# Optimization experiments

Measured on AMD Instinct MI355X. Metric: run time of the kernel, lower is better.

Reference implementation:

```python
import jax, jax.numpy as jnp
import numpy as np

N, D, DB, E, H = 1024, 512, 64, 32768, 1024

def setup_inputs() -> dict:
    key = jax.random.key(0)
    k = jax.random.split(key, 6)
    object_feats = jax.random.normal(k[0], (N, D), dtype=jnp.float32)
    bboxes_embedding = jax.random.normal(k[1], (N, N, DB), dtype=jnp.float32)
    pairs = jax.random.randint(k[2], (E, 2), 0, N, dtype=jnp.int64)
    # Kaiming-normal-ish init for the two Linear layers
    W1 = jax.random.normal(k[3], (D + D + DB, H), dtype=jnp.float32) * np.sqrt(2.0 / (D + D + DB))
    b1 = jnp.zeros((H,), dtype=jnp.float32)
    W2 = jax.random.normal(k[4], (H, D), dtype=jnp.float32) * np.sqrt(2.0 / H)
    b2 = jnp.zeros((D,), dtype=jnp.float32)
    return {"object_feats": object_feats, "bboxes_embedding": bboxes_embedding,
            "pairs": pairs, "W1": W1, "b1": b1, "W2": W2, "b2": b2}

def reference(object_feats, bboxes_embedding, pairs, W1, b1, W2, b2):
    sub = pairs[:, 0]
    obj = pairs[:, 1]
    # gather pair features: [E, D] each, plus pairwise bbox embedding [E, DB]
    f_sub = object_feats[sub]
    f_obj = object_feats[obj]
    bb = bboxes_embedding[sub, obj]
    x = jnp.concatenate((f_sub, f_obj, bb), axis=1)  # [E, 2D+DB]
    h = jax.nn.relu(x @ W1 + b1)
    out = h @ W2 + b2  # [E, D]
    n = object_feats.shape[0]
    # scatter-mean into subject nodes; each node's own feature is included once,
    # so new_feat[i] = (object_feats[i] + sum_{pairs with sub==i} out) / (1 + count[i]).
    # Nodes with no incident pairs keep their original feature (count==0 -> identity).
    seg_sum = jax.ops.segment_sum(out, sub, num_segments=n)  # [N, D]
    count = jax.ops.segment_sum(jnp.ones((out.shape[0],), dtype=out.dtype), sub, num_segments=n)
    new_feats = (object_feats + seg_sum) / (1.0 + count)[:, None]
    return (new_feats, bboxes_embedding, pairs)
```

## Files before the change

### kernel.cpp

```cpp
#include <hip/hip_runtime.h>

#define N_OBJ 1024
#define E_P   32768

typedef float f32x4 __attribute__((ext_vector_type(4)));
typedef short bf16x8 __attribute__((ext_vector_type(8)));
typedef unsigned short u16x4 __attribute__((ext_vector_type(4)));

__device__ __forceinline__ unsigned short f2bf(float f) {
    unsigned u = __float_as_uint(f);
    u = u + 0x7FFFu + ((u >> 16) & 1u);
    return (unsigned short)(u >> 16);
}

#define OFF_A    0
#define LEN_A    2097152
#define OFF_SCAN (OFF_A + LEN_A)
#define LEN_SCAN 1048576
#define OFF_PQ   (OFF_SCAN + LEN_SCAN)
#define LEN_PQ   3145728
#define OFF_SEG  (OFF_PQ + LEN_PQ)
#define LEN_SEG  7340032
#define OFF_OUT  (OFF_SEG + LEN_SEG)
#define LEN_OUT  3145728

__device__ __forceinline__ void copy_role(const float4* __restrict__ src,
                                          float4* __restrict__ dst,
                                          int off, int len, int nb, int cb) {
    int stride = nb * 256;
    int i = off + cb * 256 + threadIdx.x;
    int end = off + len;
    for (; i + stride < end; i += 2 * stride) {
        float4 a = src[i];
        float4 b = src[i + stride];
        dst[i] = a;
        dst[i + stride] = b;
    }
    if (i < end) dst[i] = src[i];
}

__global__ __launch_bounds__(256) void k_a(const float* __restrict__ W1,
                                           const float* __restrict__ W2,
                                           const float* __restrict__ feats,
                                           const int* __restrict__ pairs,
                                           unsigned short* __restrict__ w1pqT,
                                           unsigned short* __restrict__ w1cT,
                                           unsigned short* __restrict__ w2T,
                                           unsigned short* __restrict__ featsb,
                                           float* __restrict__ out_pairs,
                                           int* __restrict__ counts,
                                           const float4* __restrict__ csrc,
                                           float4* __restrict__ cdst) {
    int bid = blockIdx.x, tid = threadIdx.x;
    if ((bid % 3) == 2) { copy_role(csrc, cdst, OFF_A, LEN_A, 1056, bid / 3); return; }
    int job = (bid / 3) * 2 + (bid % 3);
    if (job >= 1856) {
        int i = (job - 1856) * 256 + tid;
        out_pairs[i] = (float)pairs[i];
        if (i < E_P) atomicAdd(&counts[pairs[2 * i]], 1);
        return;
    }
    if (job >= 1600) {
        int base = (job - 1600) * 2048 + tid * 8;
        float4 v0 = *(const float4*)&feats[base];
        float4 v1 = *(const float4*)&feats[base + 4];
        u16x4 o0 = { f2bf(v0.x), f2bf(v0.y), f2bf(v0.z), f2bf(v0.w) };
        u16x4 o1 = { f2bf(v1.x), f2bf(v1.y), f2bf(v1.z), f2bf(v1.w) };
        *(u16x4*)&featsb[base] = o0;
        *(u16x4*)&featsb[base + 4] = o1;
        return;
    }
    const float* in; unsigned short* out;
    int LDI, LDO, r0, c0, nbase, kbase;
    if (job < 1024) {
        r0 = (job >> 5) * 32; c0 = (job & 31) * 32;
        in = W1; LDI = 1024; out = w1pqT; LDO = 512;
        nbase = c0 + (r0 >= 512 ? 1024 : 0); kbase = r0 & 511;
    } else if (job < 1088) {
        int t = job - 1024; r0 = 1024 + (t >> 5) * 32; c0 = (t & 31) * 32;
        in = W1; LDI = 1024; out = w1cT; LDO = 64;
        nbase = c0; kbase = r0 - 1024;
    } else {
        int t = job - 1088; r0 = (t >> 4) * 32; c0 = (t & 15) * 32;
        in = W2; LDI = 512; out = w2T; LDO = 1024;
        nbase = c0; kbase = r0;
    }
    __shared__ float lds[32][33];
    int ti = tid >> 3, tj = (tid & 7) * 4;
    float4 v = *(const float4*)&in[(size_t)(r0 + ti) * LDI + c0 + tj];
    lds[ti][tj] = v.x; lds[ti][tj + 1] = v.y; lds[ti][tj + 2] = v.z; lds[ti][tj + 3] = v.w;
    __syncthreads();
    int oc = tid >> 3, oj = (tid & 7) * 4;
    u16x4 o = { f2bf(lds[oj][oc]), f2bf(lds[oj + 1][oc]),
                f2bf(lds[oj + 2][oc]), f2bf(lds[oj + 3][oc]) };
    *(u16x4*)&out[(size_t)(nbase + oc) * LDO + kbase + oj] = o;
}

__global__ __launch_bounds__(256) void k_scan(const int* __restrict__ counts,
                                              int* __restrict__ cursor,
                                              unsigned* __restrict__ brec,
                                              int* __restrict__ bcnt,
                                              const float4* __restrict__ csrc,
                                              float4* __restrict__ cdst) {
    int bid = blockIdx.x, tid = threadIdx.x;
    if (bid != 0) { copy_role(csrc, cdst, OFF_SCAN, LEN_SCAN, 1024, bid - 1); return; }
    __shared__ int buf[2][256];
    int c[4]; int s = 0;
    #pragma unroll
    for (int i = 0; i < 4; ++i) { c[i] = counts[tid * 4 + i]; s += c[i]; }
    buf[0][tid] = s;
    __syncthreads();
    int sel = 0;
    for (int d = 1; d < 256; d <<= 1) {
        int v = buf[sel][tid];
        if (tid >= d) v += buf[sel][tid - d];
        buf[sel ^ 1][tid] = v;
        sel ^= 1;
        __syncthreads();
    }
    int base = buf[sel][tid] - s;
    int run = base;
    #pragma unroll
    for (int i = 0; i < 4; ++i) { cursor[tid * 4 + i] = run; run += c[i]; }
    int nb[4]; int t = 0;
    #pragma unroll
    for (int i = 0; i < 4; ++i) { nb[i] = (c[i] + 31) >> 5; t += nb[i]; }
    __syncthreads();
    buf[0][tid] = t;
    __syncthreads();
    sel = 0;
    for (int d = 1; d < 256; d <<= 1) {
        int v = buf[sel][tid];
        if (tid >= d) v += buf[sel][tid - d];
        buf[sel ^ 1][tid] = v;
        sel ^= 1;
        __syncthreads();
    }
    int bpos = buf[sel][tid] - t;
    int run2 = base;
    #pragma unroll
    for (int i = 0; i < 4; ++i) {
        int seg = tid * 4 + i;
        for (int k = 0; k < nb[i]; ++k) {
            int st = run2 + k * 32;
            int cnt = c[i] - k * 32; if (cnt > 32) cnt = 32;
            brec[bpos++] = (unsigned)st | ((unsigned)seg << 16) | ((unsigned)(cnt - 1) << 26);
        }
        run2 += c[i];
    }
    if (tid == 255) bcnt[0] = bpos;
}

__global__ __launch_bounds__(256) void k_pq(const unsigned short* __restrict__ featsb,
                                            const unsigned short* __restrict__ w1pqT,
                                            const float* __restrict__ b1,
                                            float* __restrict__ P, float* __restrict__ Q,
                                            const int* __restrict__ pairs,
                                            int* __restrict__ cursor,
                                            int* __restrict__ csr_obj,
                                            const float4* __restrict__ csrc,
                                            float4* __restrict__ cdst) {
    int bid = blockIdx.x;
    if (bid >= 1536) {
        int e = (bid - 1536) * 256 + threadIdx.x;
        int sidx = pairs[2 * e];
        int pos = atomicAdd(&cursor[sidx], 1);
        csr_obj[pos] = pairs[2 * e + 1];
        return;
    }
    if ((bid % 3) < 2) { copy_role(csrc, cdst, OFF_PQ, LEN_PQ, 1024, (bid / 3) * 2 + (bid % 3)); return; }
    int job = bid / 3;
    int m0 = (job >> 5) * 64, n0 = (job & 31) * 64;
    int tid = threadIdx.x, w = tid >> 6, l = tid & 63;
    int ln = l & 15, kb = (l >> 4) * 8;
    int row = m0 + w * 16 + ln;
    f32x4 acc[4] = {};
    for (int k0 = 0; k0 < 512; k0 += 32) {
        bf16x8 a = *(const bf16x8*)&featsb[(size_t)row * 512 + k0 + kb];
        #pragma unroll
        for (int f = 0; f < 4; ++f) {
            bf16x8 b = *(const bf16x8*)&w1pqT[(size_t)(n0 + f * 16 + ln) * 512 + k0 + kb];
            acc[f] = __builtin_amdgcn_mfma_f32_16x16x32_bf16(a, b, acc[f], 0, 0, 0);
        }
    }
    int mr = m0 + w * 16 + (l >> 4) * 4;
    if (n0 < 1024) {
        #pragma unroll
        for (int f = 0; f < 4; ++f) {
            int n = n0 + f * 16 + ln;
            float b1v = b1[n];
            #pragma unroll
            for (int r = 0; r < 4; ++r)
                P[(size_t)(mr + r) * 1024 + n] = acc[f][r] + b1v;
        }
    } else {
        #pragma unroll
        for (int f = 0; f < 4; ++f) {
            int n = n0 - 1024 + f * 16 + ln;
            #pragma unroll
            for (int r = 0; r < 4; ++r)
                Q[(size_t)(mr + r) * 1024 + n] = acc[f][r];
        }
    }
}

__global__ __launch_bounds__(256) void k_seg(const int* __restrict__ csr_obj,
                                             const unsigned* __restrict__ brec,
                                             const int* __restrict__ bcnt,
                                             const float* __restrict__ bb,
                                             const unsigned short* __restrict__ w1cT,
                                             const float* __restrict__ P,
                                             const float* __restrict__ Q,
                                             float* __restrict__ HS,
                                             const float4* __restrict__ csrc,
                                             float4* __restrict__ cdst) {
    int bid = blockIdx.x;
    if ((bid % 2) == 0) { copy_role(csrc, cdst, OFF_SEG, LEN_SEG, 2048, bid / 2); return; }
    int b = bid / 2;
    if (b >= bcnt[0]) return;
    unsigned rec = brec[b];
    const int start = rec & 0xFFFF;
    const int seg = (rec >> 16) & 0x3FF;
    const int n = ((rec >> 26) & 31) + 1;

    const int tid = threadIdx.x, w = tid >> 6, l = tid & 63;
    const int ln = l & 15, g4 = l >> 4, kb = g4 * 8;
    const int n0 = w * 256;
    const int nA = n < 16 ? n : 16;
    const int nB = n - 16;

    int iA = start + (ln < nA ? ln : nA - 1);
    int iB = (nB > 0) ? (start + 16 + (ln < nB ? ln : nB - 1)) : iA;
    int objA = csr_obj[iA];
    int objB = csr_obj[iB];

    const float* brA = &bb[((size_t)seg * 1024 + (size_t)objA) * 64];
    const float* brB = &bb[((size_t)seg * 1024 + (size_t)objB) * 64];
    float4 a0 = *(const float4*)&brA[kb];
    float4 a1 = *(const float4*)&brA[kb + 4];
    float4 a2 = *(const float4*)&brA[32 + kb];
    float4 a3 = *(const float4*)&brA[32 + kb + 4];
    float4 c0 = *(const float4*)&brB[kb];
    float4 c1 = *(const float4*)&brB[kb + 4];
    float4 c2 = *(const float4*)&brB[32 + kb];
    float4 c3 = *(const float4*)&brB[32 + kb + 4];
    bf16x8 A0a, A1a, A0b, A1b;
    A0a[0] = (short)f2bf(a0.x); A0a[1] = (short)f2bf(a0.y); A0a[2] = (short)f2bf(a0.z); A0a[3] = (short)f2bf(a0.w);
    A0a[4] = (short)f2bf(a1.x); A0a[5] = (short)f2bf(a1.y); A0a[6] = (short)f2bf(a1.z); A0a[7] = (short)f2bf(a1.w);
    A1a[0] = (short)f2bf(a2.x); A1a[1] = (short)f2bf(a2.y); A1a[2] = (short)f2bf(a2.z); A1a[3] = (short)f2bf(a2.w);
    A1a[4] = (short)f2bf(a3.x); A1a[5] = (short)f2bf(a3.y); A1a[6] = (short)f2bf(a3.z); A1a[7] = (short)f2bf(a3.w);
    A0b[0] = (short)f2bf(c0.x); A0b[1] = (short)f2bf(c0.y); A0b[2] = (short)f2bf(c0.z); A0b[3] = (short)f2bf(c0.w);
    A0b[4] = (short)f2bf(c1.x); A0b[5] = (short)f2bf(c1.y); A0b[6] = (short)f2bf(c1.z); A0b[7] = (short)f2bf(c1.w);
    A1b[0] = (short)f2bf(c2.x); A1b[1] = (short)f2bf(c2.y); A1b[2] = (short)f2bf(c2.z); A1b[3] = (short)f2bf(c2.w);
    A1b[4] = (short)f2bf(c3.x); A1b[5] = (short)f2bf(c3.y); A1b[6] = (short)f2bf(c3.z); A1b[7] = (short)f2bf(c3.w);

    int raA0 = __shfl(objA, g4 * 4 + 0), raA1 = __shfl(objA, g4 * 4 + 1);
    int raA2 = __shfl(objA, g4 * 4 + 2), raA3 = __shfl(objA, g4 * 4 + 3);
    int raB0 = __shfl(objB, g4 * 4 + 0), raB1 = __shfl(objB, g4 * 4 + 1);
    int raB2 = __shfl(objB, g4 * 4 + 2), raB3 = __shfl(objB, g4 * 4 + 3);
    bool vA0 = (g4 * 4 + 0) < nA, vA1 = (g4 * 4 + 1) < nA;
    bool vA2 = (g4 * 4 + 2) < nA, vA3 = (g4 * 4 + 3) < nA;
    bool vB0 = (g4 * 4 + 0) < nB, vB1 = (g4 * 4 + 1) < nB;
    bool vB2 = (g4 * 4 + 2) < nB, vB3 = (g4 * 4 + 3) < nB;

    #pragma unroll 4
    for (int f = 0; f < 16; ++f) {
        int col = n0 + f * 16 + ln;
        const unsigned short* wr = &w1cT[(size_t)col * 64];
        bf16x8 b0 = *(const bf16x8*)&wr[kb];
        bf16x8 b1 = *(const bf16x8*)&wr[32 + kb];
        f32x4 dA = {0.f, 0.f, 0.f, 0.f};
        dA = __builtin_amdgcn_mfma_f32_16x16x32_bf16(A0a, b0, dA, 0, 0, 0);
        dA = __builtin_amdgcn_mfma_f32_16x16x32_bf16(A1a, b1, dA, 0, 0, 0);
        f32x4 dB = {0.f, 0.f, 0.f, 0.f};
        dB = __builtin_amdgcn_mfma_f32_16x16x32_bf16(A0b, b0, dB, 0, 0, 0);
        dB = __builtin_amdgcn_mfma_f32_16x16x32_bf16(A1b, b1, dB, 0, 0, 0);
        float pv = P[(size_t)seg * 1024 + col];
        float qA0 = Q[(size_t)raA0 * 1024 + col];
        float qA1 = Q[(size_t)raA1 * 1024 + col];
        float qA2 = Q[(size_t)raA2 * 1024 + col];
        float qA3 = Q[(size_t)raA3 * 1024 + col];
        float qB0 = Q[(size_t)raB0 * 1024 + col];
        float qB1 = Q[(size_t)raB1 * 1024 + col];
        float qB2 = Q[(size_t)raB2 * 1024 + col];
        float qB3 = Q[(size_t)raB3 * 1024 + col];
        float h = 0.f;
        h += vA0 ? fmaxf(dA[0] + pv + qA0, 0.f) : 0.f;
        h += vA1 ? fmaxf(dA[1] + pv + qA1, 0.f) : 0.f;
        h += vA2 ? fmaxf(dA[2] + pv + qA2, 0.f) : 0.f;
        h += vA3 ? fmaxf(dA[3] + pv + qA3, 0.f) : 0.f;
        h += vB0 ? fmaxf(dB[0] + pv + qB0, 0.f) : 0.f;
        h += vB1 ? fmaxf(dB[1] + pv + qB1, 0.f) : 0.f;
        h += vB2 ? fmaxf(dB[2] + pv + qB2, 0.f) : 0.f;
        h += vB3 ? fmaxf(dB[3] + pv + qB3, 0.f) : 0.f;
        h += __shfl_xor(h, 16);
        h += __shfl_xor(h, 32);
        if (l < 16) atomicAdd(&HS[(size_t)seg * 1024 + n0 + f * 16 + l], h);
    }
}

__global__ __launch_bounds__(256) void k_out(const float* __restrict__ HS,
                                             const unsigned short* __restrict__ w2T,
                                             const float* __restrict__ feats,
                                             const float* __restrict__ b2,
                                             const int* __restrict__ counts,
                                             float* __restrict__ out0,
                                             const float4* __restrict__ csrc,
                                             float4* __restrict__ cdst) {
    int bid = blockIdx.x;
    if ((bid % 9) != 8) { copy_role(csrc, cdst, OFF_OUT, LEN_OUT, 1024, (bid / 9) * 8 + (bid % 9)); return; }
    int job = bid / 9;
    int m0 = (job >> 3) * 64, n0 = (job & 7) * 64;
    int tid = threadIdx.x, w = tid >> 6, l = tid & 63;
    int ln = l & 15, kb = (l >> 4) * 8;
    int row = m0 + w * 16 + ln;
    f32x4 acc[4] = {};
    for (int k0 = 0; k0 < 1024; k0 += 32) {
        const float* hp = &HS[(size_t)row * 1024 + k0 + kb];
        float4 h0 = *(const float4*)&hp[0];
        float4 h1 = *(const float4*)&hp[4];
        bf16x8 a;
        a[0] = (short)f2bf(h0.x); a[1] = (short)f2bf(h0.y); a[2] = (short)f2bf(h0.z); a[3] = (short)f2bf(h0.w);
        a[4] = (short)f2bf(h1.x); a[5] = (short)f2bf(h1.y); a[6] = (short)f2bf(h1.z); a[7] = (short)f2bf(h1.w);
        #pragma unroll
        for (int f = 0; f < 4; ++f) {
            bf16x8 b = *(const bf16x8*)&w2T[(size_t)(n0 + f * 16 + ln) * 1024 + k0 + kb];
            acc[f] = __builtin_amdgcn_mfma_f32_16x16x32_bf16(a, b, acc[f], 0, 0, 0);
        }
    }
    int mr = m0 + w * 16 + (l >> 4) * 4;
    float cv[4], inv[4];
    #pragma unroll
    for (int r = 0; r < 4; ++r) {
        float c = (float)counts[mr + r];
        cv[r] = c;
        inv[r] = 1.0f / (1.0f + c);
    }
    #pragma unroll
    for (int f = 0; f < 4; ++f) {
        int n = n0 + f * 16 + ln;
        float b2v = b2[n];
        #pragma unroll
        for (int r = 0; r < 4; ++r) {
            float fv = feats[(size_t)(mr + r) * 512 + n];
            out0[(size_t)(mr + r) * 512 + n] = (fv + acc[f][r] + cv[r] * b2v) * inv[r];
        }
    }
}

extern "C" void kernel_launch(void* const* d_in, const int* in_sizes, int n_in,
                              void* d_out, int out_size, void* d_ws, size_t ws_size,
                              hipStream_t stream) {
    const float* feats = (const float*)d_in[0];
    const float* bb    = (const float*)d_in[1];
    const int*   pairs = (const int*)d_in[2];
    const float* W1    = (const float*)d_in[3];
    const float* b1    = (const float*)d_in[4];
    const float* W2    = (const float*)d_in[5];
    const float* b2    = (const float*)d_in[6];

    float* out        = (float*)d_out;
    float* out_feats  = out;
    float* out_bb     = out + (size_t)N_OBJ * 512;
    float* out_pairs  = out + (size_t)N_OBJ * 512 + (size_t)N_OBJ * N_OBJ * 64;

    char* w = (char*)d_ws;
    unsigned short* featsb = (unsigned short*)w;
    unsigned short* w1pqT  = (unsigned short*)(w + (1u << 20));
    float*          HS     = (float*)w;
    unsigned short* w1cT   = (unsigned short*)(w + (4u << 20));
    unsigned short* w2T    = (unsigned short*)(w + (4u << 20) + (128u << 10));
    float* P = (float*)(w + (5u << 20) + (128u << 10));
    float* Q = (float*)(w + (9u << 20) + (128u << 10));
    char* ints = w + (13u << 20) + (128u << 10);
    int*      counts  = (int*)ints;
    int*      cursor  = (int*)(ints + 4096);
    int*      csr_obj = (int*)(ints + 8192);
    unsigned* brec    = (unsigned*)(ints + 8192 + 131072);
    int*      bcnt    = (int*)(ints + 8192 + 131072 + 16384);

    const float4* cbb  = (const float4*)bb;
    float4*       cobb = (float4*)out_bb;

    hipMemsetAsync(counts, 0, 4096, stream);

    k_a<<<3168, 256, 0, stream>>>(W1, W2, feats, pairs, w1pqT, w1cT, w2T, featsb,
                                  out_pairs, counts, cbb, cobb);
    k_scan<<<1025, 256, 0, stream>>>(counts, cursor, brec, bcnt, cbb, cobb);
    k_pq<<<1664, 256, 0, stream>>>(featsb, w1pqT, b1, P, Q, pairs, cursor, csr_obj, cbb, cobb);

    hipMemsetAsync(HS, 0, (size_t)N_OBJ * 1024 * sizeof(float), stream);

    k_seg<<<4096, 256, 0, stream>>>(csr_obj, brec, bcnt, bb, w1cT, P, Q, HS, cbb, cobb);
    k_out<<<1152, 256, 0, stream>>>(HS, w2T, feats, b2, counts, out_feats, cbb, cobb);
}
```

Before: 230.5 us.

## Merge scan, CSR fill and PQ GEMM into one kernel using atomic ranks

Records each pair's rank within its subject segment when counting in the first kernel. Every CSR-fill block then recomputes the prefix scan locally and scatters directly, without a second atomic pass. This lets the scan, CSR build and P/Q GEMM run in a single launch, removing one kernel boundary and rebalancing the bbox copy slices. The cost is redundant scans in 128 blocks and an extra rank buffer.

```diff
diff --git a/kernel.cpp b/kernel.cpp
--- a/kernel.cpp
+++ b/kernel.cpp
@@ -15,14 +15,12 @@
 
 #define OFF_A    0
 #define LEN_A    2097152
-#define OFF_SCAN (OFF_A + LEN_A)
-#define LEN_SCAN 1048576
-#define OFF_PQ   (OFF_SCAN + LEN_SCAN)
-#define LEN_PQ   3145728
-#define OFF_SEG  (OFF_PQ + LEN_PQ)
-#define LEN_SEG  7340032
+#define OFF_B    (OFF_A + LEN_A)
+#define LEN_B    2621440
+#define OFF_SEG  (OFF_B + LEN_B)
+#define LEN_SEG  9437184
 #define OFF_OUT  (OFF_SEG + LEN_SEG)
-#define LEN_OUT  3145728
+#define LEN_OUT  2621440
 
 __device__ __forceinline__ void copy_role(const float4* __restrict__ src,
                                           float4* __restrict__ dst,
@@ -49,6 +47,7 @@
                                            unsigned short* __restrict__ featsb,
                                            float* __restrict__ out_pairs,
                                            int* __restrict__ counts,
+                                           int* __restrict__ rank,
                                            const float4* __restrict__ csrc,
                                            float4* __restrict__ cdst) {
     int bid = blockIdx.x, tid = threadIdx.x;
@@ -57,7 +56,7 @@
     if (job >= 1856) {
         int i = (job - 1856) * 256 + tid;
         out_pairs[i] = (float)pairs[i];
-        if (i < E_P) atomicAdd(&counts[pairs[2 * i]], 1);
+        if (i < E_P) rank[i] = atomicAdd(&counts[pairs[2 * i]], 1);
         return;
     }
     if (job >= 1600) {
@@ -96,47 +95,103 @@
     *(u16x4*)&out[(size_t)(nbase + oc) * LDO + kbase + oj] = o;
 }
 
-__global__ __launch_bounds__(256) void k_scan(const int* __restrict__ counts,
-                                              int* __restrict__ cursor,
-                                              unsigned* __restrict__ brec,
-                                              int* __restrict__ bcnt,
-                                              const float4* __restrict__ csrc,
-                                              float4* __restrict__ cdst) {
+__global__ __launch_bounds__(256) void k_b(const int* __restrict__ counts,
+                                           const int* __restrict__ rank,
+                                           const int* __restrict__ pairs,
+                                           int* __restrict__ csr_obj,
+                                           unsigned* __restrict__ brec,
+                                           int* __restrict__ bcnt,
+                                           const unsigned short* __restrict__ featsb,
+                                           const unsigned short* __restrict__ w1pqT,
+                                           const float* __restrict__ b1,
+                                           float* __restrict__ P, float* __restrict__ Q,
+                                           const float4* __restrict__ csrc,
+                                           float4* __restrict__ cdst) {
     int bid = blockIdx.x, tid = threadIdx.x;
-    if (bid != 0) { copy_role(csrc, cdst, OFF_SCAN, LEN_SCAN, 1024, bid - 1); return; }
-    __shared__ int buf[2][256];
+    if ((bid & 1) == 0) { copy_role(csrc, cdst, OFF_B, LEN_B, 672, bid >> 1); return; }
+    int role = bid >> 1;
+    if (role >= 641) return;
+
+    if (role >= 129) {
+        int job = role - 129;
+        int m0 = (job >> 5) * 64, n0 = (job & 31) * 64;
+        int w = tid >> 6, l = tid & 63;
+        int ln = l & 15, kb = (l >> 4) * 8;
+        int row = m0 + w * 16 + ln;
+        f32x4 acc[4] = {};
+        for (int k0 = 0; k0 < 512; k0 += 32) {
+            bf16x8 a = *(const bf16x8*)&featsb[(size_t)row * 512 + k0 + kb];
+            #pragma unroll
+            for (int f = 0; f < 4; ++f) {
+                bf16x8 b = *(const bf16x8*)&w1pqT[(size_t)(n0 + f * 16 + ln) * 512 + k0 + kb];
+                acc[f] = __builtin_amdgcn_mfma_f32_16x16x32_bf16(a, b, acc[f], 0, 0, 0);
+            }
+        }
+        int mr = m0 + w * 16 + (l >> 4) * 4;
+        if (n0 < 1024) {
+            #pragma unroll
+            for (int f = 0; f < 4; ++f) {
+                int n = n0 + f * 16 + ln;
+                float b1v = b1[n];
+                #pragma unroll
+                for (int r = 0; r < 4; ++r)
+                    P[(size_t)(mr + r) * 1024 + n] = acc[f][r] + b1v;
+            }
+        } else {
+            #pragma unroll
+            for (int f = 0; f < 4; ++f) {
+                int n = n0 - 1024 + f * 16 + ln;
+                #pragma unroll
+                for (int r = 0; r < 4; ++r)
+                    Q[(size_t)(mr + r) * 1024 + n] = acc[f][r];
+            }
+        }
+        return;
+    }
+
+    __shared__ int sbuf[2][256];
+    __shared__ int soff[1024];
     int c[4]; int s = 0;
     #pragma unroll
     for (int i = 0; i < 4; ++i) { c[i] = counts[tid * 4 + i]; s += c[i]; }
-    buf[0][tid] = s;
+    sbuf[0][tid] = s;
     __syncthreads();
     int sel = 0;
     for (int d = 1; d < 256; d <<= 1) {
-        int v = buf[sel][tid];
-        if (tid >= d) v += buf[sel][tid - d];
-        buf[sel ^ 1][tid] = v;
+        int v = sbuf[sel][tid];
+        if (tid >= d) v += sbuf[sel][tid - d];
+        sbuf[sel ^ 1][tid] = v;
         sel ^= 1;
         __syncthreads();
     }
-    int base = buf[sel][tid] - s;
+    int base = sbuf[sel][tid] - s;
     int run = base;
     #pragma unroll
-    for (int i = 0; i < 4; ++i) { cursor[tid * 4 + i] = run; run += c[i]; }
+    for (int i = 0; i < 4; ++i) { soff[tid * 4 + i] = run; run += c[i]; }
+    __syncthreads();
+
+    if (role >= 1) {
+        int e = (role - 1) * 256 + tid;
+        int sub = pairs[2 * e];
+        csr_obj[soff[sub] + rank[e]] = pairs[2 * e + 1];
+        return;
+    }
+
     int nb[4]; int t = 0;
     #pragma unroll
     for (int i = 0; i < 4; ++i) { nb[i] = (c[i] + 31) >> 5; t += nb[i]; }
     __syncthreads();
-    buf[0][tid] = t;
+    sbuf[0][tid] = t;
     __syncthreads();
     sel = 0;
     for (int d = 1; d < 256; d <<= 1) {
-        int v = buf[sel][tid];
-        if (tid >= d) v += buf[sel][tid - d];
-        buf[sel ^ 1][tid] = v;
+        int v = sbuf[sel][tid];
+        if (tid >= d) v += sbuf[sel][tid - d];
+        sbuf[sel ^ 1][tid] = v;
         sel ^= 1;
         __syncthreads();
     }
-    int bpos = buf[sel][tid] - t;
+    int bpos = sbuf[sel][tid] - t;
     int run2 = base;
     #pragma unroll
     for (int i = 0; i < 4; ++i) {
@@ -149,59 +204,6 @@
         run2 += c[i];
     }
     if (tid == 255) bcnt[0] = bpos;
-}
-
-__global__ __launch_bounds__(256) void k_pq(const unsigned short* __restrict__ featsb,
-                                            const unsigned short* __restrict__ w1pqT,
-                                            const float* __restrict__ b1,
-                                            float* __restrict__ P, float* __restrict__ Q,
-                                            const int* __restrict__ pairs,
-                                            int* __restrict__ cursor,
-                                            int* __restrict__ csr_obj,
-                                            const float4* __restrict__ csrc,
-                                            float4* __restrict__ cdst) {
-    int bid = blockIdx.x;
-    if (bid >= 1536) {
-        int e = (bid - 1536) * 256 + threadIdx.x;
-        int sidx = pairs[2 * e];
-        int pos = atomicAdd(&cursor[sidx], 1);
-        csr_obj[pos] = pairs[2 * e + 1];
-        return;
-    }
-    if ((bid % 3) < 2) { copy_role(csrc, cdst, OFF_PQ, LEN_PQ, 1024, (bid / 3) * 2 + (bid % 3)); return; }
-    int job = bid / 3;
-    int m0 = (job >> 5) * 64, n0 = (job & 31) * 64;
-    int tid = threadIdx.x, w = tid >> 6, l = tid & 63;
-    int ln = l & 15, kb = (l >> 4) * 8;
-    int row = m0 + w * 16 + ln;
-    f32x4 acc[4] = {};
-    for (int k0 = 0; k0 < 512; k0 += 32) {
-        bf16x8 a = *(const bf16x8*)&featsb[(size_t)row * 512 + k0 + kb];
-        #pragma unroll
-        for (int f = 0; f < 4; ++f) {
-            bf16x8 b = *(const bf16x8*)&w1pqT[(size_t)(n0 + f * 16 + ln) * 512 + k0 + kb];
-            acc[f] = __builtin_amdgcn_mfma_f32_16x16x32_bf16(a, b, acc[f], 0, 0, 0);
-        }
-    }
-    int mr = m0 + w * 16 + (l >> 4) * 4;
-    if (n0 < 1024) {
-        #pragma unroll
-        for (int f = 0; f < 4; ++f) {
-            int n = n0 + f * 16 + ln;
-            float b1v = b1[n];
-            #pragma unroll
-            for (int r = 0; r < 4; ++r)
-                P[(size_t)(mr + r) * 1024 + n] = acc[f][r] + b1v;
-        }
-    } else {
-        #pragma unroll
-        for (int f = 0; f < 4; ++f) {
-            int n = n0 - 1024 + f * 16 + ln;
-            #pragma unroll
-            for (int r = 0; r < 4; ++r)
-                Q[(size_t)(mr + r) * 1024 + n] = acc[f][r];
-        }
-    }
 }
 
 __global__ __launch_bounds__(256) void k_seg(const int* __restrict__ csr_obj,
@@ -374,10 +376,10 @@
     float* Q = (float*)(w + (9u << 20) + (128u << 10));
     char* ints = w + (13u << 20) + (128u << 10);
     int*      counts  = (int*)ints;
-    int*      cursor  = (int*)(ints + 4096);
-    int*      csr_obj = (int*)(ints + 8192);
-    unsigned* brec    = (unsigned*)(ints + 8192 + 131072);
-    int*      bcnt    = (int*)(ints + 8192 + 131072 + 16384);
+    int*      csr_obj = (int*)(ints + 4096);
+    unsigned* brec    = (unsigned*)(ints + 4096 + 131072);
+    int*      bcnt    = (int*)(ints + 4096 + 131072 + 16384);
+    int*      rank    = (int*)(ints + 4096 + 131072 + 16384 + 64);
 
     const float4* cbb  = (const float4*)bb;
     float4*       cobb = (float4*)out_bb;
@@ -385,9 +387,9 @@
     hipMemsetAsync(counts, 0, 4096, stream);
 
     k_a<<<3168, 256, 0, stream>>>(W1, W2, feats, pairs, w1pqT, w1cT, w2T, featsb,
-                                  out_pairs, counts, cbb, cobb);
-    k_scan<<<1025, 256, 0, stream>>>(counts, cursor, brec, bcnt, cbb, cobb);
-    k_pq<<<1664, 256, 0, stream>>>(featsb, w1pqT, b1, P, Q, pairs, cursor, csr_obj, cbb, cobb);
+                                  out_pairs, counts, rank, cbb, cobb);
+    k_b<<<1344, 256, 0, stream>>>(counts, rank, pairs, csr_obj, brec, bcnt,
+                                  featsb, w1pqT, b1, P, Q, cbb, cobb);
 
     hipMemsetAsync(HS, 0, (size_t)N_OBJ * 1024 * sizeof(float), stream);
 
```

Measured after the change: 229.7 us. No clear change (-0.3%).
